# Performance work log

Measured on AMD Instinct MI355X. Metric: run time of the kernel, lower is better.

Reference implementation:

```python
import jax, jax.numpy as jnp
import numpy as np

D_MODEL = 1024
NUM_HEADS = 16
D_K = D_MODEL // NUM_HEADS
THETA = 10000.0


def _rope(x, pos):
    # x: [B, H, S, D_K], pos: [S]
    angles = 1.0 / (THETA ** (jnp.arange(0, D_K, 2, dtype=jnp.float32) / D_K))  # [D_K/2]
    ang = pos.astype(jnp.float32)[:, None] * angles  # [S, D_K/2]
    cos = jnp.repeat(jnp.cos(ang), 2, axis=-1)  # [S, D_K]
    sin = jnp.repeat(jnp.sin(ang), 2, axis=-1)
    x2 = x.reshape(*x.shape[:-1], D_K // 2, 2)
    xr = jnp.stack([-x2[..., 1], x2[..., 0]], axis=-1).reshape(x.shape)
    return x * cos + xr * sin


def setup_inputs() -> dict:
    key = jax.random.key(0)
    ks = jax.random.split(key, 5)
    B, S = 2, 2048
    sd = np.sqrt(2.0 / (D_MODEL + D_MODEL))
    return {
        "x": jax.random.normal(ks[0], (B, S, D_MODEL), dtype=jnp.float32),
        "token_positions": jnp.arange(S, dtype=jnp.int32),
        "Wq": jax.random.normal(ks[1], (D_MODEL, D_MODEL), dtype=jnp.float32) * sd,
        "Wk": jax.random.normal(ks[2], (D_MODEL, D_MODEL), dtype=jnp.float32) * sd,
        "Wv": jax.random.normal(ks[3], (D_MODEL, D_MODEL), dtype=jnp.float32) * sd,
        "Wo": jax.random.normal(ks[4], (D_MODEL, D_MODEL), dtype=jnp.float32) * sd,
    }


def reference(x, token_positions, Wq, Wk, Wv, Wo):
    B, S, _ = x.shape

    def proj_heads(W):
        y = jnp.einsum('bsd,ed->bse', x, W)  # weight stored [d_out, d_in]
        return y.reshape(B, S, NUM_HEADS, D_K).transpose(0, 2, 1, 3)  # [B,H,S,Dk]

    q = _rope(proj_heads(Wq), token_positions)
    k = _rope(proj_heads(Wk), token_positions)
    v = proj_heads(Wv)

    scores = jnp.einsum('bhqd,bhkd->bhqk', q, k) / np.sqrt(D_K)  # [B,H,S,S]
    causal = jnp.tril(jnp.ones((S, S), dtype=bool))
    scores = jnp.where(causal, scores, -jnp.inf)
    attn = jax.nn.softmax(scores, axis=-1)
    out = jnp.einsum('bhqk,bhkd->bhqd', attn, v)  # [B,H,S,Dk]
    out = out.transpose(0, 2, 1, 3).reshape(B, S, D_MODEL)
    return jnp.einsum('bsd,ed->bse', out, Wo)
```

## Files before the change

### kernel.cpp

```cpp
#include <hip/hip_runtime.h>
#include <hip/hip_bf16.h>
#include <cstdint>
#include <cmath>

#define SEQ 2048
#define NH 16
#define DM 1024
#define BATCH 2

typedef short bf16x8 __attribute__((ext_vector_type(8)));
typedef float f32x4 __attribute__((ext_vector_type(4)));
typedef const void __attribute__((address_space(1)))* gas_t;
typedef void __attribute__((address_space(3)))* las_t;

#if __has_builtin(__builtin_amdgcn_exp2f)
#define EXP2(x) __builtin_amdgcn_exp2f(x)
#else
#define EXP2(x) __expf((x) * 0.6931471805599453f)
#endif

#define QSCALE 0.18033688011112042f

static __device__ __forceinline__ unsigned short f2bf(float f) {
    union { __hip_bfloat16 h; unsigned short u; } cv;
    cv.h = __float2bfloat16(f);
    return cv.u;
}
static __device__ __forceinline__ float bf2f(unsigned short u) {
    union { unsigned short u; __hip_bfloat16 h; } cv;
    cv.u = u;
    return __bfloat162float(cv.h);
}

static __device__ __forceinline__ void gload_lds16(const void* g, void* l) {
    __builtin_amdgcn_global_load_lds(
        reinterpret_cast<gas_t>(reinterpret_cast<uintptr_t>(g)),
        reinterpret_cast<las_t>(reinterpret_cast<uintptr_t>(l)),
        16, 0, 0);
}

static __device__ __forceinline__ unsigned ldsoff(const void* p) {
    return (unsigned)(uintptr_t)p;
}
static __device__ __forceinline__ bf16x8 dsr128(unsigned off) {
    bf16x8 r;
    asm volatile("ds_read_b128 %0, %1" : "=v"(r) : "v"(off));
    return r;
}
#define LGKM0_FENCE() do { \
    asm volatile("s_waitcnt lgkmcnt(0)" ::: "memory"); \
    __builtin_amdgcn_sched_barrier(0); \
} while (0)

__global__ __launch_bounds__(256) void cvt_all(
    const float* __restrict__ x,  const float* __restrict__ wq,
    const float* __restrict__ wk, const float* __restrict__ wv,
    const float* __restrict__ wo,
    unsigned short* __restrict__ xb, unsigned short* __restrict__ wqkv,
    unsigned short* __restrict__ wob) {
    int blk = blockIdx.x;
    const float* src; unsigned short* dst; int base;
    if (blk < 4096)      { src = x;  dst = xb;              base = blk; }
    else if (blk < 5120) { src = wq; dst = wqkv;            base = blk - 4096; }
    else if (blk < 6144) { src = wk; dst = wqkv + 1048576;  base = blk - 5120; }
    else if (blk < 7168) { src = wv; dst = wqkv + 2097152;  base = blk - 6144; }
    else                 { src = wo; dst = wob;             base = blk - 7168; }
    int i = base * 256 + threadIdx.x;
    float4 v = reinterpret_cast<const float4*>(src)[i];
    ushort4 o;
    o.x = f2bf(v.x); o.y = f2bf(v.y); o.z = f2bf(v.z); o.w = f2bf(v.w);
    reinterpret_cast<ushort4*>(dst)[i] = o;
}

template<int OUT_BF16>
__global__ __launch_bounds__(256) void gemm_bt(
    const unsigned short* __restrict__ A,
    const unsigned short* __restrict__ B,
    void* __restrict__ C, int M, int N, int K) {
    __shared__ unsigned short As[128 * 32];
    __shared__ unsigned short Bs[128 * 32];
    const int tid = threadIdx.x;
    const int lane = tid & 63, wid = tid >> 6;
    const int wr = wid >> 1, wc = wid & 1;
    const int ln15 = lane & 15, kq = lane >> 4;
    const int bm = blockIdx.y, bn = blockIdx.x;

    f32x4 acc[4][4] = {};
    const int nk = K >> 5;
    for (int kt = 0; kt < nk; ++kt) {
        #pragma unroll
        for (int i = 0; i < 2; ++i) {
            int c = i * 256 + tid;
            int row = c >> 2, k8 = (c & 3) << 3;
            size_t gofsA = (size_t)(bm * 128 + row) * K + kt * 32 + k8;
            size_t gofsB = (size_t)(bn * 128 + row) * K + kt * 32 + k8;
            unsigned ldsoff_ = (unsigned)(i * 256 + wid * 64) * 16;
            gload_lds16(A + gofsA, (char*)As + ldsoff_);
            gload_lds16(B + gofsB, (char*)Bs + ldsoff_);
        }
        __syncthreads();
        bf16x8 af[4], bf[4];
        #pragma unroll
        for (int m = 0; m < 4; ++m)
            af[m] = *reinterpret_cast<const bf16x8*>(&As[(wr * 64 + m * 16 + ln15) * 32 + kq * 8]);
        #pragma unroll
        for (int n = 0; n < 4; ++n)
            bf[n] = *reinterpret_cast<const bf16x8*>(&Bs[(wc * 64 + n * 16 + ln15) * 32 + kq * 8]);
        #pragma unroll
        for (int m = 0; m < 4; ++m)
            #pragma unroll
            for (int n = 0; n < 4; ++n)
                acc[m][n] = __builtin_amdgcn_mfma_f32_16x16x32_bf16(af[m], bf[n], acc[m][n], 0, 0, 0);
        __syncthreads();
    }
    #pragma unroll
    for (int m = 0; m < 4; ++m) {
        #pragma unroll
        for (int n = 0; n < 4; ++n) {
            int col = bn * 128 + wc * 64 + n * 16 + ln15;
            #pragma unroll
            for (int j = 0; j < 4; ++j) {
                int row = bm * 128 + wr * 64 + m * 16 + kq * 4 + j;
                if constexpr (OUT_BF16 != 0)
                    ((unsigned short*)C)[(size_t)row * N + col] = f2bf(acc[m][n][j]);
                else
                    ((float*)C)[(size_t)row * N + col] = acc[m][n][j];
            }
        }
    }
}

__global__ __launch_bounds__(512) void gemm256_bt(
    const unsigned short* __restrict__ A,
    const unsigned short* __restrict__ B,
    unsigned short* __restrict__ Qh, unsigned short* __restrict__ Kh,
    unsigned short* __restrict__ Vtr, const float2* __restrict__ tab, int K) {
    __shared__ unsigned short As[2][256 * 64];
    __shared__ unsigned short Bs[2][192 * 64];
    const int tid = threadIdx.x;
    const int lane = tid & 63, wid = tid >> 6;
    const int wm = wid >> 2, wn = wid & 3;
    const int ln15 = lane & 15, g = lane >> 4;
    const int bid = blockIdx.x;
    const int xcd = bid & 7, lid = bid >> 3;
    const int bm = (xcd >> 1) * 4 + (lid & 3);
    const int bn = (xcd & 1) * 8 + (lid >> 2);

    const unsigned short* aSrc[4];
    #pragma unroll
    for (int p = 0; p < 4; ++p) {
        int c = tid + (p << 9);
        int row = c >> 3, slot = c & 7;
        aSrc[p] = A + (size_t)(bm * 256 + row) * K + ((slot ^ (row & 7)) << 3);
    }
    const unsigned short* bSrc[3];
    #pragma unroll
    for (int u = 0; u < 3; ++u) {
        int c = tid + (u << 9);
        int row = c >> 3, slot = c & 7;
        bSrc[u] = B + (size_t)(bn * 192 + row) * K + ((slot ^ (row & 7)) << 3);
    }
    auto stageA = [&](int kt, int h) {
        #pragma unroll
        for (int p = 2 * h; p < 2 * h + 2; ++p) {
            unsigned dst = (unsigned)(tid + (p << 9)) << 4;
            gload_lds16(aSrc[p] + kt * 64, (char*)As[kt & 1] + dst);
        }
    };
    auto stageB1 = [&](int kt, int u) {
        unsigned dst = (unsigned)(tid + (u << 9)) << 4;
        gload_lds16(bSrc[u] + kt * 64, (char*)Bs[kt & 1] + dst);
    };

    const unsigned ps0 = (unsigned)((g ^ (ln15 & 7)) << 4);
    const unsigned ps1 = (unsigned)(((4 + g) ^ (ln15 & 7)) << 4);
    const unsigned aBase = (unsigned)(wm * 128 + ln15) * 128;
    const unsigned bBase = (unsigned)(wn * 48 + ln15) * 128;
    const unsigned asO[2] = { ldsoff(As[0]), ldsoff(As[1]) };
    const unsigned bsO[2] = { ldsoff(Bs[0]), ldsoff(Bs[1]) };

    f32x4 acc[8][3] = {};
    const int nkt = K >> 6;
    const int nit = nkt >> 1;

    stageA(0, 0); stageA(0, 1);
    stageB1(0, 0); stageB1(0, 1); stageB1(0, 2);
    stageB1(1, 0); stageB1(1, 1); stageB1(1, 2);
    asm volatile("s_waitcnt vmcnt(3)" ::: "memory");
    __builtin_amdgcn_s_barrier();

    for (int j = 0; j < nit; ++j) {
        const int t0 = 2 * j, t1 = 2 * j + 1;
        const bool more = (t0 + 2) < nkt;
        #pragma unroll
        for (int grp = 0; grp < 2; ++grp) {
            const unsigned aOffG = asO[grp] + aBase;
            const unsigned bOffG = bsO[grp] + bBase;
            bf16x8 bfr[3][2];
            #pragma unroll
            for (int q = 0; q < 4; ++q) {
                if (q == 0) {
                    #pragma unroll
                    for (int nf = 0; nf < 3; ++nf) {
                        bfr[nf][0] = dsr128(bOffG + nf * 2048 + ps0);
                        bfr[nf][1] = dsr128(bOffG + nf * 2048 + ps1);
                    }
                }
                bf16x8 af0 = dsr128(aOffG + (2 * q) * 2048 + ps0);
                bf16x8 af1 = dsr128(aOffG + (2 * q) * 2048 + ps1);
                bf16x8 af2 = dsr128(aOffG + (2 * q + 1) * 2048 + ps0);
                bf16x8 af3 = dsr128(aOffG + (2 * q + 1) * 2048 + ps1);

                if (grp == 0) {
                    if (q == 0) stageA(t1, 0);
                    else if (q == 1) stageA(t1, 1);
                    else if (q == 2) { if (more) { stageB1(t0 + 2, 0); stageB1(t0 + 2, 1); } }
                    else {
                        if (more) { stageB1(t0 + 2, 2);
                                    asm volatile("s_waitcnt vmcnt(3)" ::: "memory"); }
                        else      { asm volatile("s_waitcnt vmcnt(0)" ::: "memory"); }
                    }
                } else {
                    if (q == 0)      { if (more) stageA(t0 + 2, 0); }
                    else if (q == 1) { if (more) stageA(t0 + 2, 1); }
                    else if (q == 2) { if (more) { stageB1(t1 + 2, 0); stageB1(t1 + 2, 1); } }
                    else {
                        if (more) { stageB1(t1 + 2, 2);
                                    asm volatile("s_waitcnt vmcnt(3)" ::: "memory"); }
                        else      { asm volatile("s_waitcnt vmcnt(0)" ::: "memory"); }
                    }
                }

                __builtin_amdgcn_s_barrier();
                LGKM0_FENCE();
                __builtin_amdgcn_s_setprio(1);
                #pragma unroll
                for (int nf = 0; nf < 3; ++nf) {
                    acc[2 * q][nf] = __builtin_amdgcn_mfma_f32_16x16x32_bf16(af0, bfr[nf][0], acc[2 * q][nf], 0, 0, 0);
                    acc[2 * q][nf] = __builtin_amdgcn_mfma_f32_16x16x32_bf16(af1, bfr[nf][1], acc[2 * q][nf], 0, 0, 0);
                    acc[2 * q + 1][nf] = __builtin_amdgcn_mfma_f32_16x16x32_bf16(af2, bfr[nf][0], acc[2 * q + 1][nf], 0, 0, 0);
                    acc[2 * q + 1][nf] = __builtin_amdgcn_mfma_f32_16x16x32_bf16(af3, bfr[nf][1], acc[2 * q + 1][nf], 0, 0, 0);
                }
                __builtin_amdgcn_s_setprio(0);
                __builtin_amdgcn_s_barrier();
            }
        }
    }

    #pragma unroll
    for (int mf = 0; mf < 8; ++mf) {
        int row0 = bm * 256 + wm * 128 + mf * 16 + g * 4;
        int b = row0 >> 11, s0 = row0 & 2047;
        #pragma unroll
        for (int nf = 0; nf < 3; ++nf) {
            int scol = bn * 192 + wn * 48 + nf * 16;
            int sel = scol >> 10;
            int c10 = scol & 1023;
            int h = c10 >> 6;
            int d = (c10 & 63) + ln15;
            if (sel == 2) {
                ushort4 w;
                w.x = f2bf(acc[mf][nf][0]); w.y = f2bf(acc[mf][nf][1]);
                w.z = f2bf(acc[mf][nf][2]); w.w = f2bf(acc[mf][nf][3]);
                *reinterpret_cast<ushort4*>(
                    &Vtr[(((size_t)(b * NH + h)) * 64 + d) * SEQ + s0]) = w;
            } else {
                unsigned short* dst = (sel == 0) ? Qh : Kh;
                const float sc = (sel == 0) ? QSCALE : 1.f;
                int i = d >> 1;
                #pragma unroll
                for (int j2 = 0; j2 < 4; ++j2) {
                    float v = acc[mf][nf][j2];
                    float p = __shfl_xor(v, 1);
                    float2 cs = tab[((s0 + j2) << 5) + i];
                    float oe = v * cs.x - p * cs.y;
                    float oo = p * cs.x + v * cs.y;
                    if (!(d & 1)) {
                        ushort2 w2;
                        w2.x = f2bf(oe * sc); w2.y = f2bf(oo * sc);
                        *reinterpret_cast<ushort2*>(
                            &dst[(((size_t)(b * NH + h)) * SEQ + (s0 + j2)) * 64 + d]) = w2;
                    }
                }
            }
        }
    }
}

__global__ __launch_bounds__(256) void rope_table(const int* __restrict__ pos,
                                                  float2* __restrict__ tab) {
    int idx = blockIdx.x * 256 + threadIdx.x;
    int s = idx >> 5, i = idx & 31;
    float fpos = (float)pos[s];
    float freq = exp2f(-(float)i * (13.287712379549449f / 32.0f));
    float ang = fpos * freq, sn, cs;
    sincosf(ang, &sn, &cs);
    tab[idx] = make_float2(cs, sn);
}

__global__ __launch_bounds__(128) void attn_kernel(
    const unsigned short* __restrict__ Qh, const unsigned short* __restrict__ Kh,
    const unsigned short* __restrict__ Vt, unsigned short* __restrict__ Out) {
    __shared__ unsigned short Kb[2][64 * 64];
    __shared__ unsigned short Vb[2][64 * 64];
    __shared__ unsigned short Plds[2][16 * 72];

    const int tid = threadIdx.x;
    const int wid = tid >> 6, lane = tid & 63;
    const int ln15 = lane & 15, g = lane >> 4;
    const int bid = blockIdx.x;
    const int bh = bid & 31;
    const int pb = bid >> 5;

    const unsigned short* Qp = Qh + (size_t)bh * SEQ * 64;
    const unsigned short* Kp = Kh + (size_t)bh * SEQ * 64;
    const unsigned short* Vp = Vt + (size_t)bh * 64 * SEQ;
    char* Pc = (char*)Plds[wid];
    const unsigned pBase = ldsoff(Plds[wid]);
    const unsigned kbO[2] = { ldsoff(Kb[0]), ldsoff(Kb[1]) };
    const unsigned vbO[2] = { ldsoff(Vb[0]), ldsoff(Vb[1]) };

    const unsigned short* kSrc[4];
    const unsigned short* vSrc[4];
    #pragma unroll
    for (int p = 0; p < 4; ++p) {
        int c = tid + (p << 7);
        int row = c >> 3, slot = c & 7;
        kSrc[p] = Kp + (size_t)row * 64 + ((slot ^ (row & 7)) << 3);
        vSrc[p] = Vp + (size_t)row * SEQ + ((slot ^ (row & 7)) << 3);
    }

    auto stage = [&](int kb, int buf) {
        #pragma unroll
        for (int p = 0; p < 4; ++p) {
            unsigned bb = (unsigned)(wid * 1024 + p * 2048);
            gload_lds16(kSrc[p] + (size_t)kb * 64, (char*)Kb[buf] + bb);
            gload_lds16(vSrc[p] + kb, (char*)Vb[buf] + bb);
        }
    };

    unsigned kOff[4][2], vOff[4][2];
    #pragma unroll
    for (int s = 0; s < 4; ++s) {
        int r = ln15 + 16 * s;
        kOff[s][0] = r * 128 + ((g ^ (r & 7)) << 4);
        kOff[s][1] = r * 128 + (((4 + g) ^ (r & 7)) << 4);
    }
    #pragma unroll
    for (int c = 0; c < 4; ++c) {
        int d = c * 16 + ln15;
        vOff[c][0] = d * 128 + ((g ^ (d & 7)) << 4);
        vOff[c][1] = d * 128 + (((4 + g) ^ (d & 7)) << 4);
    }
    const unsigned pW = (unsigned)(ln15 * 144 + 8 * g);
    const unsigned pR = (unsigned)(ln15 * 144 + 16 * g);

    const int b = bh >> 4, h = bh & 15;

    for (int bi = 0; bi < 2; ++bi) {
        const int bnd = bi ? (63 - pb) : pb;
        const int qb = bnd * 32 + wid * 16;
        const int nt = (bnd + 2) >> 1;
        const int thr = qb + ln15 - 4 * g;

        bf16x8 aq0 = *reinterpret_cast<const bf16x8*>(Qp + (size_t)(qb + ln15) * 64 + g * 8);
        bf16x8 aq1 = *reinterpret_cast<const bf16x8*>(Qp + (size_t)(qb + ln15) * 64 + 32 + g * 8);

        f32x4 oacc[4] = {};
        float lsum = 0.f;

        stage(0, 0);

        for (int t = 0; t < nt; ++t) {
            const int kb = t << 6;
            const int cur = t & 1;
            if (t + 1 < nt) {
                stage((t + 1) << 6, cur ^ 1);
                asm volatile("s_waitcnt vmcnt(8)" ::: "memory");
            } else {
                asm volatile("s_waitcnt vmcnt(0)" ::: "memory");
            }
            __builtin_amdgcn_s_barrier();

            const unsigned kB = kbO[cur], vB = vbO[cur];
            bf16x8 kf[8], bv[8];
            #pragma unroll
            for (int s = 0; s < 4; ++s) {
                kf[2 * s]     = dsr128(kB + kOff[s][0]);
                kf[2 * s + 1] = dsr128(kB + kOff[s][1]);
            }
            #pragma unroll
            for (int c = 0; c < 4; ++c) {
                bv[2 * c]     = dsr128(vB + vOff[c][0]);
                bv[2 * c + 1] = dsr128(vB + vOff[c][1]);
            }
            LGKM0_FENCE();

            const f32x4 z = {};
            f32x4 sq[4];
            #pragma unroll
            for (int s = 0; s < 4; ++s) {
                sq[s] = __builtin_amdgcn_mfma_f32_16x16x32_bf16(kf[2 * s], aq0, z, 0, 0, 0);
                sq[s] = __builtin_amdgcn_mfma_f32_16x16x32_bf16(kf[2 * s + 1], aq1, sq[s], 0, 0, 0);
            }

            float pv[4][4];
            if (t == nt - 1) {
                #pragma unroll
                for (int s = 0; s < 4; ++s)
                    #pragma unroll
                    for (int j = 0; j < 4; ++j)
                        pv[s][j] = (j <= thr - kb - 16 * s) ? EXP2(sq[s][j]) : 0.f;
            } else {
                #pragma unroll
                for (int s = 0; s < 4; ++s)
                    #pragma unroll
                    for (int j = 0; j < 4; ++j)
                        pv[s][j] = EXP2(sq[s][j]);
            }
            #pragma unroll
            for (int s = 0; s < 4; ++s)
                lsum += (pv[s][0] + pv[s][1]) + (pv[s][2] + pv[s][3]);

            #pragma unroll
            for (int s = 0; s < 4; ++s) {
                ushort4 w;
                w.x = f2bf(pv[s][0]); w.y = f2bf(pv[s][1]);
                w.z = f2bf(pv[s][2]); w.w = f2bf(pv[s][3]);
                *reinterpret_cast<ushort4*>(Pc + pW + 32 * s) = w;
            }
            LGKM0_FENCE();
            bf16x8 ap0 = dsr128(pBase + pR);
            bf16x8 ap1 = dsr128(pBase + pR + 64);
            LGKM0_FENCE();
            #pragma unroll
            for (int c = 0; c < 4; ++c) {
                oacc[c] = __builtin_amdgcn_mfma_f32_16x16x32_bf16(ap0, bv[2 * c], oacc[c], 0, 0, 0);
                oacc[c] = __builtin_amdgcn_mfma_f32_16x16x32_bf16(ap1, bv[2 * c + 1], oacc[c], 0, 0, 0);
            }
            __builtin_amdgcn_s_barrier();
        }

        float r = lsum;
        r += __shfl_xor(r, 16);
        r += __shfl_xor(r, 32);
        float linv = 1.f / r;
        float invj[4];
        #pragma unroll
        for (int j = 0; j < 4; ++j)
            invj[j] = __shfl(linv, 20 * g + j);
        #pragma unroll
        for (int c = 0; c < 4; ++c)
            #pragma unroll
            for (int j = 0; j < 4; ++j) {
                int s = qb + g * 4 + j;
                Out[((size_t)(b * SEQ + s)) * DM + h * 64 + c * 16 + ln15] =
                    f2bf(oacc[c][j] * invj[j]);
            }
    }
}

extern "C" void kernel_launch(void* const* d_in, const int* in_sizes, int n_in,
                              void* d_out, int out_size, void* d_ws, size_t ws_size,
                              hipStream_t stream) {
    const float* x = (const float*)d_in[0];
    const int* pos = (const int*)d_in[1];
    const float* Wq = (const float*)d_in[2];
    const float* Wk = (const float*)d_in[3];
    const float* Wv = (const float*)d_in[4];
    const float* Wo = (const float*)d_in[5];
    float* out = (float*)d_out;

    char* ws = (char*)d_ws;
    const size_t MB = 1024 * 1024;
    unsigned short* xb   = (unsigned short*)(ws + 0 * MB);
    unsigned short* wqkv = (unsigned short*)(ws + 8 * MB);
    unsigned short* wob  = (unsigned short*)(ws + 14 * MB);
    float2*         tab  = (float2*)       (ws + 40 * MB);
    unsigned short* qh   = (unsigned short*)(ws + 41 * MB);
    unsigned short* kh   = (unsigned short*)(ws + 49 * MB);
    unsigned short* vtr  = (unsigned short*)(ws + 57 * MB);
    unsigned short* att  = (unsigned short*)(ws + 65 * MB);

    cvt_all<<<8192, 256, 0, stream>>>(x, Wq, Wk, Wv, Wo, xb, wqkv, wob);
    rope_table<<<256, 256, 0, stream>>>(pos, tab);

    gemm256_bt<<<256, 512, 0, stream>>>(xb, wqkv, qh, kh, vtr, tab, 1024);

    attn_kernel<<<1024, 128, 0, stream>>>(qh, kh, vtr, att);

    gemm_bt<0><<<dim3(8, 32), 256, 0, stream>>>(att, wob, out, 4096, 1024, 1024);
}
```

Measured before the change: 126.5 us.

## Replace pipelined 256x192 QKV GEMM with simple 128x128 single-buffered kernel

```diff
diff --git a/kernel.cpp b/kernel.cpp
--- a/kernel.cpp
+++ b/kernel.cpp
@@ -130,138 +130,61 @@
     }
 }
 
-__global__ __launch_bounds__(512) void gemm256_bt(
+__global__ __launch_bounds__(256) void gemm_qkv(
     const unsigned short* __restrict__ A,
     const unsigned short* __restrict__ B,
     unsigned short* __restrict__ Qh, unsigned short* __restrict__ Kh,
     unsigned short* __restrict__ Vtr, const float2* __restrict__ tab, int K) {
-    __shared__ unsigned short As[2][256 * 64];
-    __shared__ unsigned short Bs[2][192 * 64];
+    __shared__ unsigned short As[128 * 32];
+    __shared__ unsigned short Bs[128 * 32];
     const int tid = threadIdx.x;
     const int lane = tid & 63, wid = tid >> 6;
-    const int wm = wid >> 2, wn = wid & 3;
-    const int ln15 = lane & 15, g = lane >> 4;
-    const int bid = blockIdx.x;
-    const int xcd = bid & 7, lid = bid >> 3;
-    const int bm = (xcd >> 1) * 4 + (lid & 3);
-    const int bn = (xcd & 1) * 8 + (lid >> 2);
-
-    const unsigned short* aSrc[4];
+    const int wr = wid >> 1, wc = wid & 1;
+    const int ln15 = lane & 15, kq = lane >> 4;
+    const int bm = blockIdx.y, bn = blockIdx.x;
+
+    f32x4 acc[4][4] = {};
+    const int nk = K >> 5;
+    for (int kt = 0; kt < nk; ++kt) {
+        #pragma unroll
+        for (int i = 0; i < 2; ++i) {
+            int c = i * 256 + tid;
+            int row = c >> 2, k8 = (c & 3) << 3;
+            size_t gofsA = (size_t)(bm * 128 + row) * K + kt * 32 + k8;
+            size_t gofsB = (size_t)(bn * 128 + row) * K + kt * 32 + k8;
+            unsigned ldsoff_ = (unsigned)(i * 256 + wid * 64) * 16;
+            gload_lds16(A + gofsA, (char*)As + ldsoff_);
+            gload_lds16(B + gofsB, (char*)Bs + ldsoff_);
+        }
+        __syncthreads();
+        bf16x8 af[4], bf[4];
+        #pragma unroll
+        for (int m = 0; m < 4; ++m)
+            af[m] = *reinterpret_cast<const bf16x8*>(&As[(wr * 64 + m * 16 + ln15) * 32 + kq * 8]);
+        #pragma unroll
+        for (int n = 0; n < 4; ++n)
+            bf[n] = *reinterpret_cast<const bf16x8*>(&Bs[(wc * 64 + n * 16 + ln15) * 32 + kq * 8]);
+        #pragma unroll
+        for (int m = 0; m < 4; ++m)
+            #pragma unroll
+            for (int n = 0; n < 4; ++n)
+                acc[m][n] = __builtin_amdgcn_mfma_f32_16x16x32_bf16(af[m], bf[n], acc[m][n], 0, 0, 0);
+        __syncthreads();
+    }
+
+    const int sel = bn >> 3;
+    const int h = (bn & 7) * 2 + wc;
     #pragma unroll
-    for (int p = 0; p < 4; ++p) {
-        int c = tid + (p << 9);
-        int row = c >> 3, slot = c & 7;
-        aSrc[p] = A + (size_t)(bm * 256 + row) * K + ((slot ^ (row & 7)) << 3);
-    }
-    const unsigned short* bSrc[3];
-    #pragma unroll
-    for (int u = 0; u < 3; ++u) {
-        int c = tid + (u << 9);
-        int row = c >> 3, slot = c & 7;
-        bSrc[u] = B + (size_t)(bn * 192 + row) * K + ((slot ^ (row & 7)) << 3);
-    }
-    auto stageA = [&](int kt, int h) {
-        #pragma unroll
-        for (int p = 2 * h; p < 2 * h + 2; ++p) {
-            unsigned dst = (unsigned)(tid + (p << 9)) << 4;
-            gload_lds16(aSrc[p] + kt * 64, (char*)As[kt & 1] + dst);
-        }
-    };
-    auto stageB1 = [&](int kt, int u) {
-        unsigned dst = (unsigned)(tid + (u << 9)) << 4;
-        gload_lds16(bSrc[u] + kt * 64, (char*)Bs[kt & 1] + dst);
-    };
-
-    const unsigned ps0 = (unsigned)((g ^ (ln15 & 7)) << 4);
-    const unsigned ps1 = (unsigned)(((4 + g) ^ (ln15 & 7)) << 4);
-    const unsigned aBase = (unsigned)(wm * 128 + ln15) * 128;
-    const unsigned bBase = (unsigned)(wn * 48 + ln15) * 128;
-    const unsigned asO[2] = { ldsoff(As[0]), ldsoff(As[1]) };
-    const unsigned bsO[2] = { ldsoff(Bs[0]), ldsoff(Bs[1]) };
-
-    f32x4 acc[8][3] = {};
-    const int nkt = K >> 6;
-    const int nit = nkt >> 1;
-
-    stageA(0, 0); stageA(0, 1);
-    stageB1(0, 0); stageB1(0, 1); stageB1(0, 2);
-    stageB1(1, 0); stageB1(1, 1); stageB1(1, 2);
-    asm volatile("s_waitcnt vmcnt(3)" ::: "memory");
-    __builtin_amdgcn_s_barrier();
-
-    for (int j = 0; j < nit; ++j) {
-        const int t0 = 2 * j, t1 = 2 * j + 1;
-        const bool more = (t0 + 2) < nkt;
-        #pragma unroll
-        for (int grp = 0; grp < 2; ++grp) {
-            const unsigned aOffG = asO[grp] + aBase;
-            const unsigned bOffG = bsO[grp] + bBase;
-            bf16x8 bfr[3][2];
-            #pragma unroll
-            for (int q = 0; q < 4; ++q) {
-                if (q == 0) {
-                    #pragma unroll
-                    for (int nf = 0; nf < 3; ++nf) {
-                        bfr[nf][0] = dsr128(bOffG + nf * 2048 + ps0);
-                        bfr[nf][1] = dsr128(bOffG + nf * 2048 + ps1);
-                    }
-                }
-                bf16x8 af0 = dsr128(aOffG + (2 * q) * 2048 + ps0);
-                bf16x8 af1 = dsr128(aOffG + (2 * q) * 2048 + ps1);
-                bf16x8 af2 = dsr128(aOffG + (2 * q + 1) * 2048 + ps0);
-                bf16x8 af3 = dsr128(aOffG + (2 * q + 1) * 2048 + ps1);
-
-                if (grp == 0) {
-                    if (q == 0) stageA(t1, 0);
-                    else if (q == 1) stageA(t1, 1);
-                    else if (q == 2) { if (more) { stageB1(t0 + 2, 0); stageB1(t0 + 2, 1); } }
-                    else {
-                        if (more) { stageB1(t0 + 2, 2);
-                                    asm volatile("s_waitcnt vmcnt(3)" ::: "memory"); }
-                        else      { asm volatile("s_waitcnt vmcnt(0)" ::: "memory"); }
-                    }
-                } else {
-                    if (q == 0)      { if (more) stageA(t0 + 2, 0); }
-                    else if (q == 1) { if (more) stageA(t0 + 2, 1); }
-                    else if (q == 2) { if (more) { stageB1(t1 + 2, 0); stageB1(t1 + 2, 1); } }
-                    else {
-                        if (more) { stageB1(t1 + 2, 2);
-                                    asm volatile("s_waitcnt vmcnt(3)" ::: "memory"); }
-                        else      { asm volatile("s_waitcnt vmcnt(0)" ::: "memory"); }
-                    }
-                }
-
-                __builtin_amdgcn_s_barrier();
-                LGKM0_FENCE();
-                __builtin_amdgcn_s_setprio(1);
-                #pragma unroll
-                for (int nf = 0; nf < 3; ++nf) {
-                    acc[2 * q][nf] = __builtin_amdgcn_mfma_f32_16x16x32_bf16(af0, bfr[nf][0], acc[2 * q][nf], 0, 0, 0);
-                    acc[2 * q][nf] = __builtin_amdgcn_mfma_f32_16x16x32_bf16(af1, bfr[nf][1], acc[2 * q][nf], 0, 0, 0);
-                    acc[2 * q + 1][nf] = __builtin_amdgcn_mfma_f32_16x16x32_bf16(af2, bfr[nf][0], acc[2 * q + 1][nf], 0, 0, 0);
-                    acc[2 * q + 1][nf] = __builtin_amdgcn_mfma_f32_16x16x32_bf16(af3, bfr[nf][1], acc[2 * q + 1][nf], 0, 0, 0);
-                }
-                __builtin_amdgcn_s_setprio(0);
-                __builtin_amdgcn_s_barrier();
-            }
-        }
-    }
-
-    #pragma unroll
-    for (int mf = 0; mf < 8; ++mf) {
-        int row0 = bm * 256 + wm * 128 + mf * 16 + g * 4;
+    for (int m = 0; m < 4; ++m) {
+        int row0 = bm * 128 + wr * 64 + m * 16 + kq * 4;
         int b = row0 >> 11, s0 = row0 & 2047;
         #pragma unroll
-        for (int nf = 0; nf < 3; ++nf) {
-            int scol = bn * 192 + wn * 48 + nf * 16;
-            int sel = scol >> 10;
-            int c10 = scol & 1023;
-            int h = c10 >> 6;
-            int d = (c10 & 63) + ln15;
+        for (int n = 0; n < 4; ++n) {
+            int d = n * 16 + ln15;
             if (sel == 2) {
                 ushort4 w;
-                w.x = f2bf(acc[mf][nf][0]); w.y = f2bf(acc[mf][nf][1]);
-                w.z = f2bf(acc[mf][nf][2]); w.w = f2bf(acc[mf][nf][3]);
+                w.x = f2bf(acc[m][n][0]); w.y = f2bf(acc[m][n][1]);
+                w.z = f2bf(acc[m][n][2]); w.w = f2bf(acc[m][n][3]);
                 *reinterpret_cast<ushort4*>(
                     &Vtr[(((size_t)(b * NH + h)) * 64 + d) * SEQ + s0]) = w;
             } else {
@@ -270,7 +193,7 @@
                 int i = d >> 1;
                 #pragma unroll
                 for (int j2 = 0; j2 < 4; ++j2) {
-                    float v = acc[mf][nf][j2];
+                    float v = acc[m][n][j2];
                     float p = __shfl_xor(v, 1);
                     float2 cs = tab[((s0 + j2) << 5) + i];
                     float oe = v * cs.x - p * cs.y;
@@ -485,7 +408,7 @@
     cvt_all<<<8192, 256, 0, stream>>>(x, Wq, Wk, Wv, Wo, xb, wqkv, wob);
     rope_table<<<256, 256, 0, stream>>>(pos, tab);
 
-    gemm256_bt<<<256, 512, 0, stream>>>(xb, wqkv, qh, kh, vtr, tab, 1024);
+    gemm_qkv<<<dim3(24, 32), 256, 0, stream>>>(xb, wqkv, qh, kh, vtr, tab, 1024);
 
     attn_kernel<<<1024, 128, 0, stream>>>(qh, kh, vtr, att);
 
```

Result: slower. 130.4 us (+3.1%).
